# Kernel tuning notes

Measured on AMD Instinct MI355X. Metric: run time of the kernel, lower is better.

The kernel has to match this reference:

```python
import jax, jax.numpy as jnp
import numpy as np

# CapsuleConv2d(128, 256, 3, in_length=16, out_length=16, stride=1, padding=1,
#               share_weight=True, routing_type='k_means' (dot), num_iterations=3, squash=True)
KH = KW = 3
SH = SW = 1
PH = PW = 1
DH = DW = 1
IN_LENGTH = 16
OUT_LENGTH = 16
NUM_ITERS = 3
EPS = 1e-12


def _extract_patches(x):
    # x: [B, C, H, W] -> [B, C, KH, KW, OH, OW] (torch.nn.functional.unfold layout)
    B, C, H, W = x.shape
    OH = (H + 2 * PH - DH * (KH - 1) - 1) // SH + 1
    OW = (W + 2 * PW - DW * (KW - 1) - 1) // SW + 1
    xp = jnp.pad(x, ((0, 0), (0, 0), (PH, PH), (PW, PW)))
    rows = []
    for i in range(KH):  # small fixed kernel loop
        cols = []
        for j in range(KW):
            cols.append(xp[:, :, i * DH: i * DH + (OH - 1) * SH + 1: SH,
                              j * DW: j * DW + (OW - 1) * SW + 1: SW])
        rows.append(jnp.stack(cols, axis=2))
    return jnp.stack(rows, axis=2)  # [B, C, KH, KW, OH, OW]


def _k_means_routing(u, num_iterations):
    # u: [B, OH, OW, N_in, O, L]; routing over N_in (axis -3), dot similarity
    v = u.mean(axis=-3, keepdims=True)  # [B, OH, OW, 1, O, L]
    for _ in range(num_iterations):
        vn = v / jnp.maximum(jnp.linalg.norm(v, axis=-1, keepdims=True), EPS)
        logits = jnp.sum(u * vn, axis=-1, keepdims=True)      # [B,OH,OW,N_in,O,1]
        probs = jax.nn.softmax(logits, axis=-3)
        v = jnp.sum(probs * u, axis=-3, keepdims=True)
    return jnp.squeeze(v, axis=-3)  # [B, OH, OW, O, L]


def _squash(s):
    norm = jnp.linalg.norm(s, axis=-1, keepdims=True)
    return s * (norm / (1.0 + norm * norm))  # = ||s||^2/(1+||s||^2) * s/||s||


def setup_inputs() -> dict:
    key = jax.random.key(0)
    k1, k2 = jax.random.split(key)
    x = jax.random.normal(k1, (2, 128, 32, 32), dtype=jnp.float32)
    # weight: [O=out_channels//out_length, L=out_length, M=in_length, KH, KW]
    fan = IN_LENGTH * KH * KW + OUT_LENGTH * KH * KW
    bound = float(np.sqrt(6.0 / fan))  # xavier_uniform-ish scale
    weight = jax.random.uniform(k2, (16, 16, 16, 3, 3), dtype=jnp.float32,
                                minval=-bound, maxval=bound)
    return {"x": x, "weight": weight}


def reference(x, weight):
    B = x.shape[0]
    O, L, M = weight.shape[0], weight.shape[1], weight.shape[2]
    patches = _extract_patches(x)                      # [B, C, KH, KW, OH, OW]
    OH, OW = patches.shape[-2], patches.shape[-1]
    G = x.shape[1] // M
    patches = patches.reshape(B, G, M, KH, KW, OH, OW)
    # priors[b,h,w,g,i,j,o,l] = sum_m patch[b,g,m,i,j,h,w] * weight[o,l,m,i,j]
    priors = jnp.einsum('bgmijhw,olmij->bhwgijol', patches, weight)
    priors = priors.reshape(B, OH, OW, G * KH * KW, O, L)
    v = _k_means_routing(priors, NUM_ITERS)            # [B, OH, OW, O, L]
    v = _squash(v)
    out = v.reshape(B, OH, OW, O * L).transpose(0, 3, 1, 2)  # [B, C_out, OH, OW]
    return out
```

## Files before the change

kernel.cpp:

```cpp
#include <hip/hip_runtime.h>


typedef float v2f __attribute__((ext_vector_type(2)));
typedef int   i4  __attribute__((ext_vector_type(4)));
typedef short bh8 __attribute__((ext_vector_type(8)));
typedef float f16v __attribute__((ext_vector_type(16)));

#define XT_ELEMS (2 * 32 * 32 * 128)
#define WBF_ELEMS (9 * 8 * 2 * 64 * 8)
#define STR 34

#define DPP_ADD(a, ctrl)                                                     \
  a += __int_as_float(__builtin_amdgcn_update_dpp(                           \
          0, __float_as_int(a), ctrl, 0xF, 0xF, true))

__device__ __forceinline__ float dpp_add16(float x) {
    float s = x;
    DPP_ADD(s, 0x128); DPP_ADD(s, 0x124); DPP_ADD(s, 0x122); DPP_ADD(s, 0x121);
    return s;
}

__device__ __forceinline__ float swz16_add(float x) {
    int y = __builtin_amdgcn_ds_swizzle(__float_as_int(x), 0x401F);
    return x + __int_as_float(y);
}

__device__ __forceinline__ float frcp(float x) {
    return __builtin_amdgcn_rcpf(x);
}

__device__ __forceinline__ v2f pkfma(v2f a, v2f b, v2f c) {
    return __builtin_elementwise_fma(a, b, c);
}

__global__ __launch_bounds__(256)
void prep_kernel(const float* __restrict__ x, const float* __restrict__ W,
                 float* __restrict__ xT, unsigned short* __restrict__ Wbf) {
    const int blk = blockIdx.x;
    const int tid = threadIdx.x;
    if (blk < 64) {
        __shared__ float xs[128 * 33];
        const int b = blk >> 5, h = blk & 31;
        const float* xb = x + b * (128 * 32 * 32) + h * 32;
        #pragma unroll
        for (int k = 0; k < 16; ++k) {
            int idx = k * 256 + tid;
            int c = idx >> 5, w = idx & 31;
            xs[c * 33 + w] = xb[c * 1024 + w];
        }
        __syncthreads();
        float* xo = xT + (b * 32 + h) * 32 * 128;
        #pragma unroll
        for (int k = 0; k < 16; ++k) {
            int idx = k * 256 + tid;
            int w = idx >> 7, c = idx & 127;
            xo[w * 128 + c] = xs[c * 33 + w];
        }
    } else {
        int idx = (blk - 64) * 256 + tid;
        int j  = idx & 7;
        int L  = (idx >> 3) & 63;
        int s  = (idx >> 9) & 1;
        int tt = (idx >> 10) & 7;
        int ij = idx >> 13;
        int k  = (L >> 5) * 8 + j;
        int t  = tt * 32 + (L & 31);
        float wv = W[(t * 16 + k) * 9 + ij];
        unsigned bits = __float_as_uint(wv);
        unsigned hib  = bits & 0xFFFF0000u;
        unsigned short val;
        if (s == 0) val = (unsigned short)(hib >> 16);
        else {
            float lo = wv - __uint_as_float(hib);
            val = (unsigned short)(__float_as_uint(lo) >> 16);
        }
        Wbf[idx] = val;
    }
}

#define CWR(REG, IJ)                                                         \
    uLds[wroff + STR * ((((REG) >> 2) * 72) + (((REG) & 3) * 9) + (IJ))] =   \
        acc[(REG)];

#define DO_IJ(IJ)                                                            \
  { const int di = (IJ) / 3, dj = (IJ) % 3;                                  \
    const int hh = h + di - 1;                                               \
    const bool hok = (unsigned)hh < 32u;                                     \
    const int hhc = hok ? hh : 0;                                            \
    const int ww = w0 + pl + dj - 1;                                         \
    const bool ok = hok && ((unsigned)ww < 32u);                             \
    const int wwc = ok ? ww : 0;                                             \
    const float* ap = xT + (((bb * 32 + hhc) * 32 + wwc) * 128               \
                            + gl * 16 + half * 8);                           \
    float f0 = ap[0], f1 = ap[1], f2 = ap[2], f3 = ap[3];                    \
    float f4 = ap[4], f5 = ap[5], f6 = ap[6], f7 = ap[7];                    \
    const float msk = ok ? 1.0f : 0.0f;                                      \
    f0 *= msk; f1 *= msk; f2 *= msk; f3 *= msk;                              \
    f4 *= msk; f5 *= msk; f6 *= msk; f7 *= msk;                              \
    unsigned b0 = __float_as_uint(f0), b1 = __float_as_uint(f1);             \
    unsigned b2 = __float_as_uint(f2), b3 = __float_as_uint(f3);             \
    unsigned b4 = __float_as_uint(f4), b5 = __float_as_uint(f5);             \
    unsigned b6 = __float_as_uint(f6), b7 = __float_as_uint(f7);             \
    i4 hp, lp;                                                               \
    hp.x = (int)((b0 >> 16) | (b1 & 0xFFFF0000u));                           \
    hp.y = (int)((b2 >> 16) | (b3 & 0xFFFF0000u));                           \
    hp.z = (int)((b4 >> 16) | (b5 & 0xFFFF0000u));                           \
    hp.w = (int)((b6 >> 16) | (b7 & 0xFFFF0000u));                           \
    unsigned l0 = __float_as_uint(f0 - __uint_as_float(b0 & 0xFFFF0000u));   \
    unsigned l1 = __float_as_uint(f1 - __uint_as_float(b1 & 0xFFFF0000u));   \
    unsigned l2 = __float_as_uint(f2 - __uint_as_float(b2 & 0xFFFF0000u));   \
    unsigned l3 = __float_as_uint(f3 - __uint_as_float(b3 & 0xFFFF0000u));   \
    unsigned l4 = __float_as_uint(f4 - __uint_as_float(b4 & 0xFFFF0000u));   \
    unsigned l5 = __float_as_uint(f5 - __uint_as_float(b5 & 0xFFFF0000u));   \
    unsigned l6 = __float_as_uint(f6 - __uint_as_float(b6 & 0xFFFF0000u));   \
    unsigned l7 = __float_as_uint(f7 - __uint_as_float(b7 & 0xFFFF0000u));   \
    lp.x = (int)((l0 >> 16) | (l1 & 0xFFFF0000u));                           \
    lp.y = (int)((l2 >> 16) | (l3 & 0xFFFF0000u));                           \
    lp.z = (int)((l4 >> 16) | (l5 & 0xFFFF0000u));                           \
    lp.w = (int)((l6 >> 16) | (l7 & 0xFFFF0000u));                           \
    i4 bhiw = bfr[((IJ) * 8 + tt) * 128 + lane];                             \
    i4 blow = bfr[((IJ) * 8 + tt) * 128 + 64 + lane];                        \
    bh8 aHi = __builtin_bit_cast(bh8, hp);                                   \
    bh8 aLo = __builtin_bit_cast(bh8, lp);                                   \
    bh8 bHi = __builtin_bit_cast(bh8, bhiw);                                 \
    bh8 bLo = __builtin_bit_cast(bh8, blow);                                 \
    f16v acc = {0.f,0.f,0.f,0.f,0.f,0.f,0.f,0.f,                             \
                0.f,0.f,0.f,0.f,0.f,0.f,0.f,0.f};                            \
    acc = __builtin_amdgcn_mfma_f32_32x32x16_bf16(aHi, bLo, acc, 0, 0, 0);   \
    acc = __builtin_amdgcn_mfma_f32_32x32x16_bf16(aLo, bHi, acc, 0, 0, 0);   \
    acc = __builtin_amdgcn_mfma_f32_32x32x16_bf16(aHi, bHi, acc, 0, 0, 0);   \
    CWR(0, IJ)  CWR(1, IJ)  CWR(2, IJ)  CWR(3, IJ)                           \
    CWR(4, IJ)  CWR(5, IJ)  CWR(6, IJ)  CWR(7, IJ)                           \
    CWR(8, IJ)  CWR(9, IJ)  CWR(10, IJ) CWR(11, IJ)                          \
    CWR(12, IJ) CWR(13, IJ) CWR(14, IJ) CWR(15, IJ) }

#define LROW(K)                                                              \
  { const v2f* r2_ = (const v2f*)(rb + (K) * 16 * STR);                      \
    U##K##0 = r2_[0]; U##K##1 = r2_[1]; U##K##2 = r2_[2]; U##K##3 = r2_[3]; }

#define DOTR(K)                                                              \
  ({ v2f d_ = U##K##0 * V0;                                                  \
     d_ = pkfma(U##K##1, V1, d_); d_ = pkfma(U##K##2, V2, d_);               \
     d_ = pkfma(U##K##3, V3, d_); swz16_add(d_.x + d_.y); })

#define MEANJ(J)                                                             \
  { v2f s_ = (U0##J + U1##J) + (U2##J + U3##J) + U4##J;                      \
    V##J.x = dpp_add16(s_.x) * (1.0f / 72.0f);                               \
    V##J.y = dpp_add16(s_.y) * (1.0f / 72.0f); }

#define UPDJ(J)                                                              \
  { v2f pv_ = e0v * U0##J;                                                   \
    pv_ = pkfma(e1v, U1##J, pv_); pv_ = pkfma(e2v, U2##J, pv_);              \
    pv_ = pkfma(e3v, U3##J, pv_); pv_ = pkfma(e4v, U4##J, pv_);              \
    V##J.x = dpp_add16(pv_.x) * rs;                                          \
    V##J.y = dpp_add16(pv_.y) * rs; }

__global__ __launch_bounds__(256, 4)
void capsule_v9(const float* __restrict__ xT,
                const unsigned short* __restrict__ Wbf,
                float* __restrict__ out) {
    __shared__ float uLds[4 * 72 * STR];
    const int blk = blockIdx.x;
    const int tt = blk & 7;
    const int q  = blk >> 3;
    const int bb = q >> 8;
    const int r  = q & 255;
    const int h  = r >> 3;
    const int w0 = (r & 7) << 2;
    const int tid = threadIdx.x;

    {
        const int lane = tid & 63;
        const int wv   = tid >> 6;
        const int pl   = (lane & 31) >> 3;
        const int gl   = lane & 7;
        const int half = lane >> 5;
        const int tl   = lane & 31;
        const int wroff = tl + STR * 9 * 4 * half;
        const i4* bfr = (const i4*)Wbf;
        if (wv == 0)      { DO_IJ(0) DO_IJ(4) DO_IJ(8) }
        else if (wv == 1) { DO_IJ(1) DO_IJ(5) }
        else if (wv == 2) { DO_IJ(2) DO_IJ(6) }
        else              { DO_IJ(3) DO_IJ(7) }
    }
    __syncthreads();

    const int p  = tid >> 6;
    const int i6 = tid & 63;
    const int o2 = i6 >> 5;
    const int jh = (i6 >> 4) & 1;
    const int sc = i6 & 15;
    const bool has5 = (sc < 8);
    const float* rb = uLds + (p * 72 + sc) * STR + o2 * 16 + jh * 8;

    v2f U00, U01, U02, U03;
    v2f U10, U11, U12, U13;
    v2f U20, U21, U22, U23;
    v2f U30, U31, U32, U33;
    v2f U40, U41, U42, U43;
    U40 = U41 = U42 = U43 = (v2f){0.0f, 0.0f};
    LROW(0) LROW(1) LROW(2) LROW(3)
    if (has5) LROW(4)

    v2f V0, V1, V2, V3;
    MEANJ(0) MEANJ(1) MEANJ(2) MEANJ(3)

    #pragma unroll 1
    for (int it = 0; it < 3; ++it) {
        v2f ssv = V0 * V0;
        ssv = pkfma(V1, V1, ssv); ssv = pkfma(V2, V2, ssv);
        ssv = pkfma(V3, V3, ssv);
        float ss = swz16_add(ssv.x + ssv.y);
        float inv = frcp(fmaxf(sqrtf(ss), 1e-12f));

        float E0 = __expf(DOTR(0) * inv);
        float E1 = __expf(DOTR(1) * inv);
        float E2 = __expf(DOTR(2) * inv);
        float E3 = __expf(DOTR(3) * inv);
        float E4 = has5 ? __expf(DOTR(4) * inv) : 0.0f;
        float ssum = dpp_add16(((E0 + E1) + (E2 + E3)) + E4);
        float rs = frcp(ssum);

        v2f e0v = {E0, E0}, e1v = {E1, E1}, e2v = {E2, E2};
        v2f e3v = {E3, E3}, e4v = {E4, E4};
        UPDJ(0) UPDJ(1) UPDJ(2) UPDJ(3)
    }

    v2f ssv = V0 * V0;
    ssv = pkfma(V1, V1, ssv); ssv = pkfma(V2, V2, ssv);
    ssv = pkfma(V3, V3, ssv);
    float ss = swz16_add(ssv.x + ssv.y);
    float scale = sqrtf(ss) * frcp(1.0f + ss);

    v2f aa0 = (sc & 4) ? V2 : V0;
    v2f aa1 = (sc & 4) ? V3 : V1;
    v2f bb0 = (sc & 2) ? aa1 : aa0;
    float res = ((sc & 1) ? bb0.y : bb0.x) * scale;
    if (sc < 8) {
        int tg = tt * 32 + o2 * 16 + jh * 8 + sc;
        out[((bb * 256 + tg) * 32 + h) * 32 + w0 + p] = res;
    }
}

__global__ __launch_bounds__(256, 1)
void capsule_fb(const float* __restrict__ x, const float* __restrict__ Wraw,
                float* __restrict__ out) {
    __shared__ float patch[9 * 128];
    const int blk = blockIdx.x;
    const int b = blk >> 10, h = (blk >> 5) & 31, w = blk & 31;
    const int t = threadIdx.x;

    const float* xb = x + b * (128 * 32 * 32);
    for (int idx = t; idx < 1152; idx += 256) {
        int c = idx / 9, ij = idx - c * 9;
        int di = ij / 3, dj = ij - di * 3;
        int hh = h + di - 1, ww = w + dj - 1;
        float v = 0.0f;
        if ((unsigned)hh < 32u && (unsigned)ww < 32u)
            v = xb[(c * 32 + hh) * 32 + ww];
        patch[ij * 128 + c] = v;
    }
    __syncthreads();

    float u[72];
    #pragma unroll
    for (int ij = 0; ij < 9; ++ij) {
        float wr[16];
        #pragma unroll
        for (int m = 0; m < 16; ++m) wr[m] = Wraw[(t * 16 + m) * 9 + ij];
        #pragma unroll
        for (int g = 0; g < 8; ++g) {
            float acc = 0.0f;
            #pragma unroll
            for (int m = 0; m < 16; ++m)
                acc = fmaf(patch[ij * 128 + g * 16 + m], wr[m], acc);
            u[g * 9 + ij] = acc;
        }
    }

    float v = 0.0f;
    #pragma unroll
    for (int n = 0; n < 72; ++n) v += u[n];
    v *= (1.0f / 72.0f);
    #pragma unroll 1
    for (int it = 0; it < 3; ++it) {
        float sg = dpp_add16(v * v);
        float vn = v * frcp(fmaxf(sqrtf(sg), 1e-12f));
        float ssum = 0.0f, vacc = 0.0f;
        #pragma unroll
        for (int n = 0; n < 72; ++n) {
            float pp = dpp_add16(u[n] * vn);
            float e = __expf(pp);
            ssum += e;
            vacc = fmaf(e, u[n], vacc);
        }
        v = vacc * frcp(ssum);
    }
    float sg = dpp_add16(v * v);
    float res = v * sqrtf(sg) * frcp(1.0f + sg);
    out[((b * 256 + t) * 32 + h) * 32 + w] = res;
}

extern "C" void kernel_launch(void* const* d_in, const int* in_sizes, int n_in,
                              void* d_out, int out_size, void* d_ws, size_t ws_size,
                              hipStream_t stream) {
    const float* x = (const float*)d_in[0];
    const float* W = (const float*)d_in[1];
    float* out = (float*)d_out;
    float* xT = (float*)d_ws;
    unsigned short* Wbf = (unsigned short*)(xT + XT_ELEMS);

    const size_t need = (size_t)XT_ELEMS * 4 + (size_t)WBF_ELEMS * 2;
    if (ws_size >= need) {
        prep_kernel<<<352, 256, 0, stream>>>(x, W, xT, Wbf);
        capsule_v9<<<4096, 256, 0, stream>>>(xT, Wbf, out);
    } else {
        capsule_fb<<<2048, 256, 0, stream>>>(x, W, out);
    }
}
```

Measured before the change: 80.70 us.

## Fuse prep kernel into main capsule kernel, reading raw x and weights directly

```diff
diff --git a/kernel.cpp b/kernel.cpp
--- a/kernel.cpp
+++ b/kernel.cpp
@@ -6,8 +6,6 @@
 typedef short bh8 __attribute__((ext_vector_type(8)));
 typedef float f16v __attribute__((ext_vector_type(16)));
 
-#define XT_ELEMS (2 * 32 * 32 * 128)
-#define WBF_ELEMS (9 * 8 * 2 * 64 * 8)
 #define STR 34
 
 #define DPP_ADD(a, ctrl)                                                     \
@@ -33,56 +31,41 @@
     return __builtin_elementwise_fma(a, b, c);
 }
 
-__global__ __launch_bounds__(256)
-void prep_kernel(const float* __restrict__ x, const float* __restrict__ W,
-                 float* __restrict__ xT, unsigned short* __restrict__ Wbf) {
-    const int blk = blockIdx.x;
-    const int tid = threadIdx.x;
-    if (blk < 64) {
-        __shared__ float xs[128 * 33];
-        const int b = blk >> 5, h = blk & 31;
-        const float* xb = x + b * (128 * 32 * 32) + h * 32;
-        #pragma unroll
-        for (int k = 0; k < 16; ++k) {
-            int idx = k * 256 + tid;
-            int c = idx >> 5, w = idx & 31;
-            xs[c * 33 + w] = xb[c * 1024 + w];
-        }
-        __syncthreads();
-        float* xo = xT + (b * 32 + h) * 32 * 128;
-        #pragma unroll
-        for (int k = 0; k < 16; ++k) {
-            int idx = k * 256 + tid;
-            int w = idx >> 7, c = idx & 127;
-            xo[w * 128 + c] = xs[c * 33 + w];
-        }
-    } else {
-        int idx = (blk - 64) * 256 + tid;
-        int j  = idx & 7;
-        int L  = (idx >> 3) & 63;
-        int s  = (idx >> 9) & 1;
-        int tt = (idx >> 10) & 7;
-        int ij = idx >> 13;
-        int k  = (L >> 5) * 8 + j;
-        int t  = tt * 32 + (L & 31);
-        float wv = W[(t * 16 + k) * 9 + ij];
-        unsigned bits = __float_as_uint(wv);
-        unsigned hib  = bits & 0xFFFF0000u;
-        unsigned short val;
-        if (s == 0) val = (unsigned short)(hib >> 16);
-        else {
-            float lo = wv - __uint_as_float(hib);
-            val = (unsigned short)(__float_as_uint(lo) >> 16);
-        }
-        Wbf[idx] = val;
-    }
-}
+#define BFRAG(BH, BL, IJ) {                                                  \
+    float q0 = uLds[wb + (IJ)];                                              \
+    float q1 = uLds[wb + (IJ) + 9];                                          \
+    float q2 = uLds[wb + (IJ) + 18];                                         \
+    float q3 = uLds[wb + (IJ) + 27];                                         \
+    float q4 = uLds[wb + (IJ) + 36];                                         \
+    float q5 = uLds[wb + (IJ) + 45];                                         \
+    float q6 = uLds[wb + (IJ) + 54];                                         \
+    float q7 = uLds[wb + (IJ) + 63];                                         \
+    unsigned d0 = __float_as_uint(q0), d1 = __float_as_uint(q1);             \
+    unsigned d2 = __float_as_uint(q2), d3 = __float_as_uint(q3);             \
+    unsigned d4 = __float_as_uint(q4), d5 = __float_as_uint(q5);             \
+    unsigned d6 = __float_as_uint(q6), d7 = __float_as_uint(q7);             \
+    BH.x = (int)((d0 >> 16) | (d1 & 0xFFFF0000u));                           \
+    BH.y = (int)((d2 >> 16) | (d3 & 0xFFFF0000u));                           \
+    BH.z = (int)((d4 >> 16) | (d5 & 0xFFFF0000u));                           \
+    BH.w = (int)((d6 >> 16) | (d7 & 0xFFFF0000u));                           \
+    unsigned e0 = __float_as_uint(q0 - __uint_as_float(d0 & 0xFFFF0000u));   \
+    unsigned e1 = __float_as_uint(q1 - __uint_as_float(d1 & 0xFFFF0000u));   \
+    unsigned e2 = __float_as_uint(q2 - __uint_as_float(d2 & 0xFFFF0000u));   \
+    unsigned e3 = __float_as_uint(q3 - __uint_as_float(d3 & 0xFFFF0000u));   \
+    unsigned e4 = __float_as_uint(q4 - __uint_as_float(d4 & 0xFFFF0000u));   \
+    unsigned e5 = __float_as_uint(q5 - __uint_as_float(d5 & 0xFFFF0000u));   \
+    unsigned e6 = __float_as_uint(q6 - __uint_as_float(d6 & 0xFFFF0000u));   \
+    unsigned e7 = __float_as_uint(q7 - __uint_as_float(d7 & 0xFFFF0000u));   \
+    BL.x = (int)((e0 >> 16) | (e1 & 0xFFFF0000u));                           \
+    BL.y = (int)((e2 >> 16) | (e3 & 0xFFFF0000u));                           \
+    BL.z = (int)((e4 >> 16) | (e5 & 0xFFFF0000u));                           \
+    BL.w = (int)((e6 >> 16) | (e7 & 0xFFFF0000u)); }
 
 #define CWR(REG, IJ)                                                         \
     uLds[wroff + STR * ((((REG) >> 2) * 72) + (((REG) & 3) * 9) + (IJ))] =   \
         acc[(REG)];
 
-#define DO_IJ(IJ)                                                            \
+#define DO_IJ(IJ, BH, BL)                                                    \
   { const int di = (IJ) / 3, dj = (IJ) % 3;                                  \
     const int hh = h + di - 1;                                               \
     const bool hok = (unsigned)hh < 32u;                                     \
@@ -90,10 +73,10 @@
     const int ww = w0 + pl + dj - 1;                                         \
     const bool ok = hok && ((unsigned)ww < 32u);                             \
     const int wwc = ok ? ww : 0;                                             \
-    const float* ap = xT + (((bb * 32 + hhc) * 32 + wwc) * 128               \
-                            + gl * 16 + half * 8);                           \
-    float f0 = ap[0], f1 = ap[1], f2 = ap[2], f3 = ap[3];                    \
-    float f4 = ap[4], f5 = ap[5], f6 = ap[6], f7 = ap[7];                    \
+    const float* ap = x + bb * 131072 + (gl * 16 + half * 8) * 1024          \
+                        + hhc * 32 + wwc;                                    \
+    float f0 = ap[0],    f1 = ap[1024], f2 = ap[2048], f3 = ap[3072];        \
+    float f4 = ap[4096], f5 = ap[5120], f6 = ap[6144], f7 = ap[7168];        \
     const float msk = ok ? 1.0f : 0.0f;                                      \
     f0 *= msk; f1 *= msk; f2 *= msk; f3 *= msk;                              \
     f4 *= msk; f5 *= msk; f6 *= msk; f7 *= msk;                              \
@@ -118,12 +101,10 @@
     lp.y = (int)((l2 >> 16) | (l3 & 0xFFFF0000u));                           \
     lp.z = (int)((l4 >> 16) | (l5 & 0xFFFF0000u));                           \
     lp.w = (int)((l6 >> 16) | (l7 & 0xFFFF0000u));                           \
-    i4 bhiw = bfr[((IJ) * 8 + tt) * 128 + lane];                             \
-    i4 blow = bfr[((IJ) * 8 + tt) * 128 + 64 + lane];                        \
     bh8 aHi = __builtin_bit_cast(bh8, hp);                                   \
     bh8 aLo = __builtin_bit_cast(bh8, lp);                                   \
-    bh8 bHi = __builtin_bit_cast(bh8, bhiw);                                 \
-    bh8 bLo = __builtin_bit_cast(bh8, blow);                                 \
+    bh8 bHi = __builtin_bit_cast(bh8, BH);                                   \
+    bh8 bLo = __builtin_bit_cast(bh8, BL);                                   \
     f16v acc = {0.f,0.f,0.f,0.f,0.f,0.f,0.f,0.f,                             \
                 0.f,0.f,0.f,0.f,0.f,0.f,0.f,0.f};                            \
     acc = __builtin_amdgcn_mfma_f32_32x32x16_bf16(aHi, bLo, acc, 0, 0, 0);   \
@@ -156,9 +137,8 @@
     V##J.y = dpp_add16(pv_.y) * rs; }
 
 __global__ __launch_bounds__(256, 4)
-void capsule_v9(const float* __restrict__ xT,
-                const unsigned short* __restrict__ Wbf,
-                float* __restrict__ out) {
+void capsule_v10(const float* __restrict__ x, const float* __restrict__ W,
+                 float* __restrict__ out) {
     __shared__ float uLds[4 * 72 * STR];
     const int blk = blockIdx.x;
     const int tt = blk & 7;
@@ -170,6 +150,16 @@
     const int tid = threadIdx.x;
 
     {
+        const float* gw = W + tt * 4608;
+        #pragma unroll
+        for (int rr = 0; rr < 18; ++rr) {
+            int i = rr * 256 + tid;
+            uLds[i + (i / 144)] = gw[i];
+        }
+    }
+    __syncthreads();
+
+    {
         const int lane = tid & 63;
         const int wv   = tid >> 6;
         const int pl   = (lane & 31) >> 3;
@@ -177,11 +167,21 @@
         const int half = lane >> 5;
         const int tl   = lane & 31;
         const int wroff = tl + STR * 9 * 4 * half;
-        const i4* bfr = (const i4*)Wbf;
-        if (wv == 0)      { DO_IJ(0) DO_IJ(4) DO_IJ(8) }
-        else if (wv == 1) { DO_IJ(1) DO_IJ(5) }
-        else if (wv == 2) { DO_IJ(2) DO_IJ(6) }
-        else              { DO_IJ(3) DO_IJ(7) }
+        const int wb = (lane & 31) * 145 + (lane >> 5) * 72;
+
+        i4 B0h = {0,0,0,0}, B0l = {0,0,0,0};
+        i4 B1h = {0,0,0,0}, B1l = {0,0,0,0};
+        i4 B2h = {0,0,0,0}, B2l = {0,0,0,0};
+        if (wv == 0)      { BFRAG(B0h,B0l,0) BFRAG(B1h,B1l,4) BFRAG(B2h,B2l,8) }
+        else if (wv == 1) { BFRAG(B0h,B0l,1) BFRAG(B1h,B1l,5) }
+        else if (wv == 2) { BFRAG(B0h,B0l,2) BFRAG(B1h,B1l,6) }
+        else              { BFRAG(B0h,B0l,3) BFRAG(B1h,B1l,7) }
+        __syncthreads();
+
+        if (wv == 0)      { DO_IJ(0,B0h,B0l) DO_IJ(4,B1h,B1l) DO_IJ(8,B2h,B2l) }
+        else if (wv == 1) { DO_IJ(1,B0h,B0l) DO_IJ(5,B1h,B1l) }
+        else if (wv == 2) { DO_IJ(2,B0h,B0l) DO_IJ(6,B1h,B1l) }
+        else              { DO_IJ(3,B0h,B0l) DO_IJ(7,B1h,B1l) }
     }
     __syncthreads();
 
@@ -242,79 +242,12 @@
     }
 }
 
-__global__ __launch_bounds__(256, 1)
-void capsule_fb(const float* __restrict__ x, const float* __restrict__ Wraw,
-                float* __restrict__ out) {
-    __shared__ float patch[9 * 128];
-    const int blk = blockIdx.x;
-    const int b = blk >> 10, h = (blk >> 5) & 31, w = blk & 31;
-    const int t = threadIdx.x;
-
-    const float* xb = x + b * (128 * 32 * 32);
-    for (int idx = t; idx < 1152; idx += 256) {
-        int c = idx / 9, ij = idx - c * 9;
-        int di = ij / 3, dj = ij - di * 3;
-        int hh = h + di - 1, ww = w + dj - 1;
-        float v = 0.0f;
-        if ((unsigned)hh < 32u && (unsigned)ww < 32u)
-            v = xb[(c * 32 + hh) * 32 + ww];
-        patch[ij * 128 + c] = v;
-    }
-    __syncthreads();
-
-    float u[72];
-    #pragma unroll
-    for (int ij = 0; ij < 9; ++ij) {
-        float wr[16];
-        #pragma unroll
-        for (int m = 0; m < 16; ++m) wr[m] = Wraw[(t * 16 + m) * 9 + ij];
-        #pragma unroll
-        for (int g = 0; g < 8; ++g) {
-            float acc = 0.0f;
-            #pragma unroll
-            for (int m = 0; m < 16; ++m)
-                acc = fmaf(patch[ij * 128 + g * 16 + m], wr[m], acc);
-            u[g * 9 + ij] = acc;
-        }
-    }
-
-    float v = 0.0f;
-    #pragma unroll
-    for (int n = 0; n < 72; ++n) v += u[n];
-    v *= (1.0f / 72.0f);
-    #pragma unroll 1
-    for (int it = 0; it < 3; ++it) {
-        float sg = dpp_add16(v * v);
-        float vn = v * frcp(fmaxf(sqrtf(sg), 1e-12f));
-        float ssum = 0.0f, vacc = 0.0f;
-        #pragma unroll
-        for (int n = 0; n < 72; ++n) {
-            float pp = dpp_add16(u[n] * vn);
-            float e = __expf(pp);
-            ssum += e;
-            vacc = fmaf(e, u[n], vacc);
-        }
-        v = vacc * frcp(ssum);
-    }
-    float sg = dpp_add16(v * v);
-    float res = v * sqrtf(sg) * frcp(1.0f + sg);
-    out[((b * 256 + t) * 32 + h) * 32 + w] = res;
-}
-
 extern "C" void kernel_launch(void* const* d_in, const int* in_sizes, int n_in,
                               void* d_out, int out_size, void* d_ws, size_t ws_size,
                               hipStream_t stream) {
     const float* x = (const float*)d_in[0];
     const float* W = (const float*)d_in[1];
     float* out = (float*)d_out;
-    float* xT = (float*)d_ws;
-    unsigned short* Wbf = (unsigned short*)(xT + XT_ELEMS);
-
-    const size_t need = (size_t)XT_ELEMS * 4 + (size_t)WBF_ELEMS * 2;
-    if (ws_size >= need) {
-        prep_kernel<<<352, 256, 0, stream>>>(x, W, xT, Wbf);
-        capsule_v9<<<4096, 256, 0, stream>>>(xT, Wbf, out);
-    } else {
-        capsule_fb<<<2048, 256, 0, stream>>>(x, W, out);
-    }
-}
+    (void)d_ws; (void)ws_size; (void)in_sizes; (void)n_in; (void)out_size;
+    capsule_v10<<<4096, 256, 0, stream>>>(x, W, out);
+}
```

Measured after the change: 86.94 us. 7.7% more time.

## Pre-split activations into bf16 hi/lo in prep and halve per-block pixel tile

Applied to the files above, without the earlier changes.

```diff
diff --git a/kernel.cpp b/kernel.cpp
--- a/kernel.cpp
+++ b/kernel.cpp
@@ -6,9 +6,9 @@
 typedef short bh8 __attribute__((ext_vector_type(8)));
 typedef float f16v __attribute__((ext_vector_type(16)));
 
-#define XT_ELEMS (2 * 32 * 32 * 128)
-#define WBF_ELEMS (9 * 8 * 2 * 64 * 8)
 #define STR 34
+#define XP_I4 65536
+#define WBF_ELEMS 73728
 
 #define DPP_ADD(a, ctrl)                                                     \
   a += __int_as_float(__builtin_amdgcn_update_dpp(                           \
@@ -34,8 +34,8 @@
 }
 
 __global__ __launch_bounds__(256)
-void prep_kernel(const float* __restrict__ x, const float* __restrict__ W,
-                 float* __restrict__ xT, unsigned short* __restrict__ Wbf) {
+void prep2_kernel(const float* __restrict__ x, const float* __restrict__ W,
+                  i4* __restrict__ xP, unsigned short* __restrict__ Wbf) {
     const int blk = blockIdx.x;
     const int tid = threadIdx.x;
     if (blk < 64) {
@@ -49,12 +49,44 @@
             xs[c * 33 + w] = xb[c * 1024 + w];
         }
         __syncthreads();
-        float* xo = xT + (b * 32 + h) * 32 * 128;
-        #pragma unroll
-        for (int k = 0; k < 16; ++k) {
-            int idx = k * 256 + tid;
-            int w = idx >> 7, c = idx & 127;
-            xo[w * 128 + c] = xs[c * 33 + w];
+        i4* xo = xP + (b * 32 + h) * 1024;
+        #pragma unroll
+        for (int it = 0; it < 4; ++it) {
+            int slot = it * 256 + tid;
+            int s  = slot & 1;
+            int hf = (slot >> 1) & 1;
+            int gl = (slot >> 2) & 7;
+            int w  = slot >> 5;
+            int c0 = gl * 16 + hf * 8;
+            float f0 = xs[(c0 + 0) * 33 + w], f1 = xs[(c0 + 1) * 33 + w];
+            float f2 = xs[(c0 + 2) * 33 + w], f3 = xs[(c0 + 3) * 33 + w];
+            float f4 = xs[(c0 + 4) * 33 + w], f5 = xs[(c0 + 5) * 33 + w];
+            float f6 = xs[(c0 + 6) * 33 + w], f7 = xs[(c0 + 7) * 33 + w];
+            unsigned b0 = __float_as_uint(f0), b1 = __float_as_uint(f1);
+            unsigned b2 = __float_as_uint(f2), b3 = __float_as_uint(f3);
+            unsigned b4 = __float_as_uint(f4), b5 = __float_as_uint(f5);
+            unsigned b6 = __float_as_uint(f6), b7 = __float_as_uint(f7);
+            i4 pk;
+            if (s == 0) {
+                pk.x = (int)((b0 >> 16) | (b1 & 0xFFFF0000u));
+                pk.y = (int)((b2 >> 16) | (b3 & 0xFFFF0000u));
+                pk.z = (int)((b4 >> 16) | (b5 & 0xFFFF0000u));
+                pk.w = (int)((b6 >> 16) | (b7 & 0xFFFF0000u));
+            } else {
+                unsigned l0 = __float_as_uint(f0 - __uint_as_float(b0 & 0xFFFF0000u));
+                unsigned l1 = __float_as_uint(f1 - __uint_as_float(b1 & 0xFFFF0000u));
+                unsigned l2 = __float_as_uint(f2 - __uint_as_float(b2 & 0xFFFF0000u));
+                unsigned l3 = __float_as_uint(f3 - __uint_as_float(b3 & 0xFFFF0000u));
+                unsigned l4 = __float_as_uint(f4 - __uint_as_float(b4 & 0xFFFF0000u));
+                unsigned l5 = __float_as_uint(f5 - __uint_as_float(b5 & 0xFFFF0000u));
+                unsigned l6 = __float_as_uint(f6 - __uint_as_float(b6 & 0xFFFF0000u));
+                unsigned l7 = __float_as_uint(f7 - __uint_as_float(b7 & 0xFFFF0000u));
+                pk.x = (int)((l0 >> 16) | (l1 & 0xFFFF0000u));
+                pk.y = (int)((l2 >> 16) | (l3 & 0xFFFF0000u));
+                pk.z = (int)((l4 >> 16) | (l5 & 0xFFFF0000u));
+                pk.w = (int)((l6 >> 16) | (l7 & 0xFFFF0000u));
+            }
+            xo[slot] = pk;
         }
     } else {
         int idx = (blk - 64) * 256 + tid;
@@ -78,61 +110,40 @@
     }
 }
 
-#define CWR(REG, IJ)                                                         \
-    uLds[wroff + STR * ((((REG) >> 2) * 72) + (((REG) & 3) * 9) + (IJ))] =   \
-        acc[(REG)];
-
-#define DO_IJ(IJ)                                                            \
-  { const int di = (IJ) / 3, dj = (IJ) % 3;                                  \
+#define ALOADIJ(AH, AL, OK, IJ) {                                            \
+    const int di = (IJ) / 3, dj = (IJ) % 3;                                  \
     const int hh = h + di - 1;                                               \
     const bool hok = (unsigned)hh < 32u;                                     \
     const int hhc = hok ? hh : 0;                                            \
     const int ww = w0 + pl + dj - 1;                                         \
-    const bool ok = hok && ((unsigned)ww < 32u);                             \
-    const int wwc = ok ? ww : 0;                                             \
-    const float* ap = xT + (((bb * 32 + hhc) * 32 + wwc) * 128               \
-                            + gl * 16 + half * 8);                           \
-    float f0 = ap[0], f1 = ap[1], f2 = ap[2], f3 = ap[3];                    \
-    float f4 = ap[4], f5 = ap[5], f6 = ap[6], f7 = ap[7];                    \
-    const float msk = ok ? 1.0f : 0.0f;                                      \
-    f0 *= msk; f1 *= msk; f2 *= msk; f3 *= msk;                              \
-    f4 *= msk; f5 *= msk; f6 *= msk; f7 *= msk;                              \
-    unsigned b0 = __float_as_uint(f0), b1 = __float_as_uint(f1);             \
-    unsigned b2 = __float_as_uint(f2), b3 = __float_as_uint(f3);             \
-    unsigned b4 = __float_as_uint(f4), b5 = __float_as_uint(f5);             \
-    unsigned b6 = __float_as_uint(f6), b7 = __float_as_uint(f7);             \
-    i4 hp, lp;                                                               \
-    hp.x = (int)((b0 >> 16) | (b1 & 0xFFFF0000u));                           \
-    hp.y = (int)((b2 >> 16) | (b3 & 0xFFFF0000u));                           \
-    hp.z = (int)((b4 >> 16) | (b5 & 0xFFFF0000u));                           \
-    hp.w = (int)((b6 >> 16) | (b7 & 0xFFFF0000u));                           \
-    unsigned l0 = __float_as_uint(f0 - __uint_as_float(b0 & 0xFFFF0000u));   \
-    unsigned l1 = __float_as_uint(f1 - __uint_as_float(b1 & 0xFFFF0000u));   \
-    unsigned l2 = __float_as_uint(f2 - __uint_as_float(b2 & 0xFFFF0000u));   \
-    unsigned l3 = __float_as_uint(f3 - __uint_as_float(b3 & 0xFFFF0000u));   \
-    unsigned l4 = __float_as_uint(f4 - __uint_as_float(b4 & 0xFFFF0000u));   \
-    unsigned l5 = __float_as_uint(f5 - __uint_as_float(b5 & 0xFFFF0000u));   \
-    unsigned l6 = __float_as_uint(f6 - __uint_as_float(b6 & 0xFFFF0000u));   \
-    unsigned l7 = __float_as_uint(f7 - __uint_as_float(b7 & 0xFFFF0000u));   \
-    lp.x = (int)((l0 >> 16) | (l1 & 0xFFFF0000u));                           \
-    lp.y = (int)((l2 >> 16) | (l3 & 0xFFFF0000u));                           \
-    lp.z = (int)((l4 >> 16) | (l5 & 0xFFFF0000u));                           \
-    lp.w = (int)((l6 >> 16) | (l7 & 0xFFFF0000u));                           \
-    i4 bhiw = bfr[((IJ) * 8 + tt) * 128 + lane];                             \
-    i4 blow = bfr[((IJ) * 8 + tt) * 128 + 64 + lane];                        \
-    bh8 aHi = __builtin_bit_cast(bh8, hp);                                   \
-    bh8 aLo = __builtin_bit_cast(bh8, lp);                                   \
-    bh8 bHi = __builtin_bit_cast(bh8, bhiw);                                 \
-    bh8 bLo = __builtin_bit_cast(bh8, blow);                                 \
+    OK = hok && ((unsigned)ww < 32u);                                        \
+    const int wwc = OK ? ww : 0;                                             \
+    const int slot = (((bb * 32 + hhc) * 32 + wwc) * 8 + gl) * 2 + half;     \
+    AH = xpi4[slot * 2]; AL = xpi4[slot * 2 + 1]; }
+
+#define BLOADIJ(BH, BL, IJ) {                                                \
+    BH = bfr[((IJ) * 8 + tt) * 128 + lane];                                  \
+    BL = bfr[((IJ) * 8 + tt) * 128 + 64 + lane]; }
+
+#define CWR(REG, IJ)                                                         \
+    uLds[wroff + STR * ((((REG) >> 2) * 72) + (((REG) & 3) * 9) + (IJ))] =   \
+        acc[(REG)];
+
+#define PROCIJ(AH, AL, OK, BH, BL, IJ) {                                     \
+    const i4 z_ = {0, 0, 0, 0};                                              \
+    i4 ah_ = OK ? AH : z_;                                                   \
+    i4 al_ = OK ? AL : z_;                                                   \
+    bh8 aHi = __builtin_bit_cast(bh8, ah_);                                  \
+    bh8 aLo = __builtin_bit_cast(bh8, al_);                                  \
+    bh8 bHi = __builtin_bit_cast(bh8, BH);                                   \
+    bh8 bLo = __builtin_bit_cast(bh8, BL);                                   \
     f16v acc = {0.f,0.f,0.f,0.f,0.f,0.f,0.f,0.f,                             \
                 0.f,0.f,0.f,0.f,0.f,0.f,0.f,0.f};                            \
     acc = __builtin_amdgcn_mfma_f32_32x32x16_bf16(aHi, bLo, acc, 0, 0, 0);   \
     acc = __builtin_amdgcn_mfma_f32_32x32x16_bf16(aLo, bHi, acc, 0, 0, 0);   \
     acc = __builtin_amdgcn_mfma_f32_32x32x16_bf16(aHi, bHi, acc, 0, 0, 0);   \
-    CWR(0, IJ)  CWR(1, IJ)  CWR(2, IJ)  CWR(3, IJ)                           \
-    CWR(4, IJ)  CWR(5, IJ)  CWR(6, IJ)  CWR(7, IJ)                           \
-    CWR(8, IJ)  CWR(9, IJ)  CWR(10, IJ) CWR(11, IJ)                          \
-    CWR(12, IJ) CWR(13, IJ) CWR(14, IJ) CWR(15, IJ) }
+    CWR(0, IJ) CWR(1, IJ) CWR(2, IJ) CWR(3, IJ)                              \
+    CWR(4, IJ) CWR(5, IJ) CWR(6, IJ) CWR(7, IJ) }
 
 #define LROW(K)                                                              \
   { const v2f* r2_ = (const v2f*)(rb + (K) * 16 * STR);                      \
@@ -155,35 +166,62 @@
     V##J.x = dpp_add16(pv_.x) * rs;                                          \
     V##J.y = dpp_add16(pv_.y) * rs; }
 
-__global__ __launch_bounds__(256, 4)
-void capsule_v9(const float* __restrict__ xT,
-                const unsigned short* __restrict__ Wbf,
-                float* __restrict__ out) {
-    __shared__ float uLds[4 * 72 * STR];
+__global__ __launch_bounds__(256, 8)
+void capsule_v12(const i4* __restrict__ xpi4, const i4* __restrict__ bfr,
+                 float* __restrict__ out) {
+    __shared__ float uLds[2 * 72 * STR];
     const int blk = blockIdx.x;
-    const int tt = blk & 7;
-    const int q  = blk >> 3;
-    const int bb = q >> 8;
-    const int r  = q & 255;
-    const int h  = r >> 3;
-    const int w0 = (r & 7) << 2;
+    const int tt  = blk & 7;
+    const int r   = blk >> 3;
+    const int bb  = r >> 9;
+    const int h   = (r >> 4) & 31;
+    const int w0  = (r & 15) << 1;
     const int tid = threadIdx.x;
 
     {
         const int lane = tid & 63;
         const int wv   = tid >> 6;
-        const int pl   = (lane & 31) >> 3;
+        const int pl   = (lane >> 3) & 1;
         const int gl   = lane & 7;
         const int half = lane >> 5;
         const int tl   = lane & 31;
         const int wroff = tl + STR * 9 * 4 * half;
-        const i4* bfr = (const i4*)Wbf;
-        if (wv == 0)      { DO_IJ(0) DO_IJ(4) DO_IJ(8) }
-        else if (wv == 1) { DO_IJ(1) DO_IJ(5) }
-        else if (wv == 2) { DO_IJ(2) DO_IJ(6) }
-        else              { DO_IJ(3) DO_IJ(7) }
+
+        if (wv == 0) {
+            i4 a0h, a0l, a1h, a1l, a2h, a2l;
+            i4 b0h, b0l, b1h, b1l, b2h, b2l;
+            bool ok0, ok1, ok2;
+            ALOADIJ(a0h, a0l, ok0, 0) BLOADIJ(b0h, b0l, 0)
+            ALOADIJ(a1h, a1l, ok1, 4) BLOADIJ(b1h, b1l, 4)
+            PROCIJ(a0h, a0l, ok0, b0h, b0l, 0)
+            ALOADIJ(a2h, a2l, ok2, 8) BLOADIJ(b2h, b2l, 8)
+            PROCIJ(a1h, a1l, ok1, b1h, b1l, 4)
+            PROCIJ(a2h, a2l, ok2, b2h, b2l, 8)
+        } else if (wv == 1) {
+            i4 a0h, a0l, a1h, a1l, b0h, b0l, b1h, b1l;
+            bool ok0, ok1;
+            ALOADIJ(a0h, a0l, ok0, 1) BLOADIJ(b0h, b0l, 1)
+            ALOADIJ(a1h, a1l, ok1, 5) BLOADIJ(b1h, b1l, 5)
+            PROCIJ(a0h, a0l, ok0, b0h, b0l, 1)
+            PROCIJ(a1h, a1l, ok1, b1h, b1l, 5)
+        } else if (wv == 2) {
+            i4 a0h, a0l, a1h, a1l, b0h, b0l, b1h, b1l;
+            bool ok0, ok1;
+            ALOADIJ(a0h, a0l, ok0, 2) BLOADIJ(b0h, b0l, 2)
+            ALOADIJ(a1h, a1l, ok1, 6) BLOADIJ(b1h, b1l, 6)
+            PROCIJ(a0h, a0l, ok0, b0h, b0l, 2)
+            PROCIJ(a1h, a1l, ok1, b1h, b1l, 6)
+        } else {
+            i4 a0h, a0l, a1h, a1l, b0h, b0l, b1h, b1l;
+            bool ok0, ok1;
+            ALOADIJ(a0h, a0l, ok0, 3) BLOADIJ(b0h, b0l, 3)
+            ALOADIJ(a1h, a1l, ok1, 7) BLOADIJ(b1h, b1l, 7)
+            PROCIJ(a0h, a0l, ok0, b0h, b0l, 3)
+            PROCIJ(a1h, a1l, ok1, b1h, b1l, 7)
+        }
     }
     __syncthreads();
+    if (tid >= 128) return;
 
     const int p  = tid >> 6;
     const int i6 = tid & 63;
@@ -307,13 +345,13 @@
     const float* x = (const float*)d_in[0];
     const float* W = (const float*)d_in[1];
     float* out = (float*)d_out;
-    float* xT = (float*)d_ws;
-    unsigned short* Wbf = (unsigned short*)(xT + XT_ELEMS);
-
-    const size_t need = (size_t)XT_ELEMS * 4 + (size_t)WBF_ELEMS * 2;
+    i4* xP = (i4*)d_ws;
+    unsigned short* Wbf = (unsigned short*)((char*)d_ws + 1048576);
+
+    const size_t need = 1048576 + (size_t)WBF_ELEMS * 2;
     if (ws_size >= need) {
-        prep_kernel<<<352, 256, 0, stream>>>(x, W, xT, Wbf);
-        capsule_v9<<<4096, 256, 0, stream>>>(xT, Wbf, out);
+        prep2_kernel<<<352, 256, 0, stream>>>(x, W, xP, Wbf);
+        capsule_v12<<<8192, 256, 0, stream>>>(xP, (const i4*)Wbf, out);
     } else {
         capsule_fb<<<2048, 256, 0, stream>>>(x, W, out);
     }
```

Result: slower. 84.51 us (+4.7%).
